# Performance work log

Hardware: AMD Instinct MI355X
Metric: run time of the kernel (lower is better)

The kernel has to match this reference:

```python
import jax, jax.numpy as jnp
import numpy as np

B, C, S, H, W = 2, 128, 64, 128, 512
MID = 32
EPS = 1e-5


def layer_norm(x, g, b):
    m = jnp.mean(x, axis=-1, keepdims=True)
    v = jnp.var(x, axis=-1, keepdims=True)
    return (x - m) / jnp.sqrt(v + EPS) * g + b


def generate_y_for_attn(s, y, u):
    # y: [B, Cy, H, W], u: [B, s, s] int indices into W (clamped)
    b, cy, h, w = y.shape
    u = jnp.clip(u, 0, w - 1)
    yr = y.reshape(b, cy * h, w)
    idx = u.reshape(b, s * s)
    g = jax.vmap(lambda m, i: m[:, i])(yr, idx)          # [B, Cy*H, s^2]
    return g.reshape(b, cy, h, s * s).transpose(0, 3, 2, 1)  # [B, s^2, H, Cy]


def setup_inputs():
    key = jax.random.key(0)
    ks = jax.random.split(key, 10)
    lim = 1.0 / np.sqrt(C)
    return {
        "sat_x": jax.random.normal(ks[0], (B, C, S, S), jnp.float32),
        "grd_x": jax.random.normal(ks[1], (B, C, H, W), jnp.float32),
        "grd_height": jax.random.normal(ks[2], (B, 1, H, W), jnp.float32),
        "u": jax.random.randint(ks[3], (B, S, S), 0, W, jnp.int32),
        "ln_q_g": jnp.ones((C,), jnp.float32),
        "ln_q_b": jnp.zeros((C,), jnp.float32),
        "wq": jax.random.uniform(ks[4], (C, MID), jnp.float32, -lim, lim),
        "bq": jax.random.uniform(ks[5], (MID,), jnp.float32, -lim, lim),
        "ln_k_g": jnp.ones((C,), jnp.float32),
        "ln_k_b": jnp.zeros((C,), jnp.float32),
        "wk": jax.random.uniform(ks[6], (C, MID), jnp.float32, -lim, lim),
        "bk": jax.random.uniform(ks[7], (MID,), jnp.float32, -lim, lim),
    }


def reference(sat_x, grd_x, grd_height, u, ln_q_g, ln_q_b, wq, bq, ln_k_g, ln_k_b, wk, bk):
    b, c, s, _ = sat_x.shape
    scale = MID ** (-0.5)
    y_attn = generate_y_for_attn(s, grd_x, u)        # [B, S^2, H, C]
    v_attn = generate_y_for_attn(s, grd_height, u)   # [B, S^2, H, 1]
    x = sat_x.reshape(b, c, s * s).transpose(0, 2, 1)  # [B, M, C]
    q = layer_norm(x, ln_q_g, ln_q_b) @ wq + bq        # [B, M, 32]
    k = layer_norm(y_attn, ln_k_g, ln_k_b) @ wk + bk   # [B, M, H, 32]
    dot = scale * jnp.einsum("bmd,bmnd->bmn", q, k)    # [B, M, H]
    att = jax.nn.softmax(dot, axis=-1)
    a = jnp.sum(att[..., None] * v_attn, axis=-2)      # [B, M, 1]
    return a.transpose(0, 2, 1).reshape(b, 1, s, s)
```

## Files before the change

### kernel.cpp

```cpp
#include <hip/hip_runtime.h>
#include <math.h>

#define B_   2
#define C_   128
#define S_   64
#define H_   128
#define W_   512
#define M_   (S_ * S_)
#define MID_ 32
#define EPS_ 1e-5f
#define CAP_ 192

#define KBLK (B_ * H_ * (W_ / 64))
#define QBLK (B_ * (M_ / 64))
#define OBLK 4

typedef __attribute__((ext_vector_type(8))) short short8;
typedef __attribute__((ext_vector_type(4))) float floatx4;

__global__ __launch_bounds__(256) void prep_kernel(
    const float* __restrict__ ln_k_g, const float* __restrict__ ln_k_b,
    const float* __restrict__ wk, const float* __restrict__ bk,
    const float* __restrict__ ln_q_g, const float* __restrict__ ln_q_b,
    const float* __restrict__ wq, const float* __restrict__ bq,
    float* __restrict__ prepbuf,
    short* __restrict__ wfrag,
    int* __restrict__ counts,
    int* __restrict__ ocount)
{
    const int tid = threadIdx.x;
    const int blk = blockIdx.x;
    const float* g    = blk ? ln_q_g : ln_k_g;
    const float* bl   = blk ? ln_q_b : ln_k_b;
    const float* wt   = blk ? wq     : wk;
    const float* bias = blk ? bq     : bk;

    __shared__ float pa[256], pb[256];

    float a = 0.f, c2 = 0.f;
#pragma unroll
    for (int k = 0; k < 16; ++k) {
        const int idx = tid + 256 * k;
        const float wv = wt[idx];
        const int c = idx >> 5;
        a  = fmaf(g[c],  wv, a);
        c2 = fmaf(bl[c], wv, c2);
    }
    pa[tid] = a; pb[tid] = c2;

    if (blk == 0) {
        ((int4*)counts)[tid] = make_int4(0, 0, 0, 0);
        if (tid == 0) *ocount = 0;
    }
    __syncthreads();

    if (tid < 32) {
        float s = 0.f, t = 0.f;
#pragma unroll
        for (int r = 0; r < 8; ++r) { s += pa[tid + 32 * r]; t += pb[tid + 32 * r]; }
        prepbuf[blk * 64 + tid]      = s;
        prepbuf[blk * 64 + 32 + tid] = t + bias[tid];
    }

    short* whiT = wfrag + blk * 8192;
    short* wloT = whiT + 4096;
#pragma unroll
    for (int e = 0; e < 16; ++e) {
        const int idx = tid * 16 + e;
        const int i    = idx & 7;
        const int ln   = (idx >> 3) & 63;
        const int kk   = (idx >> 9) & 3;
        const int jt   = idx >> 11;
        const int c = kk * 32 + (ln >> 4) * 8 + i;
        const int j = jt * 16 + (ln & 15);
        const float wp = g[c] * wt[c * MID_ + j];
        const unsigned bbits = __float_as_uint(wp);
        const unsigned hb = bbits & 0xFFFF0000u;
        whiT[idx] = (short)(hb >> 16);
        const float r = wp - __uint_as_float(hb);
        wloT[idx] = (short)(__float_as_uint(r) >> 16);
    }
}

__global__ __launch_bounds__(256) void proj_kernel(
    const float* __restrict__ grd_x,
    const float* __restrict__ sat_x,
    const float* __restrict__ prepbuf,
    const short* __restrict__ wfrag,
    const int*   __restrict__ u,
    float* __restrict__ kw,
    float* __restrict__ qv,
    int* __restrict__ counts,
    int* __restrict__ bucket,
    int* __restrict__ ocount,
    int* __restrict__ olist)
{
    const int tid  = threadIdx.x;
    const int lane = tid & 63;
    const int wv   = __builtin_amdgcn_readfirstlane(tid >> 6);
    const int quad = lane >> 4;
    const int l16  = lane & 15;
    const int blk  = blockIdx.x;
    const bool is_k = (blk < KBLK);

    int b, h = 0, pos0;
    const float* xcol;
    size_t xstr;
    if (is_k) {
        const int wchunk = blk & 7;
        h    = (blk >> 3) & (H_ - 1);
        b    = blk >> 10;
        pos0 = wchunk * 64;
        xcol = grd_x + ((size_t)b * C_ * H_ + h) * W_ + pos0;
        xstr = (size_t)H_ * W_;
    } else {
        const int qblk = blk - KBLK;
        b    = qblk >> 6;
        pos0 = (qblk & 63) * 64;
        xcol = sat_x + (size_t)b * C_ * M_ + pos0;
        xstr = (size_t)M_;
    }
    const int pos = pos0 + wv * 16 + l16;

    const float* xp = xcol + (size_t)(quad * 8) * xstr + wv * 16 + l16;
    float xv[32];
#pragma unroll
    for (int kk = 0; kk < 4; ++kk)
#pragma unroll
        for (int i = 0; i < 8; ++i)
            xv[kk * 8 + i] = xp[(size_t)(kk * 32 + i) * xstr];

    const short* whiT = wfrag + (is_k ? 0 : 8192);
    const short* wloT = whiT + 4096;
    short8 ahi[2][4], alo[2][4];
#pragma unroll
    for (int jt = 0; jt < 2; ++jt)
#pragma unroll
        for (int kk = 0; kk < 4; ++kk) {
            const int off = ((jt * 4 + kk) * 64 + lane) * 8;
            ahi[jt][kk] = *(const short8*)(whiT + off);
            alo[jt][kk] = *(const short8*)(wloT + off);
        }

    const int setoff = is_k ? 0 : 64;
    const float4 gw0 = *(const float4*)(prepbuf + setoff + quad * 4);
    const float4 bw0 = *(const float4*)(prepbuf + setoff + 32 + quad * 4);
    const float4 gw1 = *(const float4*)(prepbuf + setoff + 16 + quad * 4);
    const float4 bw1 = *(const float4*)(prepbuf + setoff + 48 + quad * 4);

    floatx4 acc0 = {0.f, 0.f, 0.f, 0.f};
    floatx4 acc1 = {0.f, 0.f, 0.f, 0.f};
    float p1 = 0.f, p2 = 0.f;

#pragma unroll
    for (int kk = 0; kk < 4; ++kk) {
        union { short8 v; unsigned u[4]; } bhi, blo;
#pragma unroll
        for (int e = 0; e < 4; ++e) {
            const float x0 = xv[kk * 8 + 2 * e];
            const float x1 = xv[kk * 8 + 2 * e + 1];
            p1 += x0 + x1;
            p2 = fmaf(x0, x0, p2);
            p2 = fmaf(x1, x1, p2);
            const unsigned b0 = __float_as_uint(x0);
            const unsigned b1 = __float_as_uint(x1);
            bhi.u[e] = (b1 & 0xFFFF0000u) | (b0 >> 16);
            const float r0 = x0 - __uint_as_float(b0 & 0xFFFF0000u);
            const float r1 = x1 - __uint_as_float(b1 & 0xFFFF0000u);
            blo.u[e] = (__float_as_uint(r1) & 0xFFFF0000u) |
                       (__float_as_uint(r0) >> 16);
        }
        acc0 = __builtin_amdgcn_mfma_f32_16x16x32_bf16(ahi[0][kk], bhi.v, acc0, 0, 0, 0);
        acc1 = __builtin_amdgcn_mfma_f32_16x16x32_bf16(ahi[1][kk], bhi.v, acc1, 0, 0, 0);
        acc0 = __builtin_amdgcn_mfma_f32_16x16x32_bf16(ahi[0][kk], blo.v, acc0, 0, 0, 0);
        acc1 = __builtin_amdgcn_mfma_f32_16x16x32_bf16(ahi[1][kk], blo.v, acc1, 0, 0, 0);
        acc0 = __builtin_amdgcn_mfma_f32_16x16x32_bf16(alo[0][kk], bhi.v, acc0, 0, 0, 0);
        acc1 = __builtin_amdgcn_mfma_f32_16x16x32_bf16(alo[1][kk], bhi.v, acc1, 0, 0, 0);
    }

    p1 += __shfl_xor(p1, 16, 64);
    p1 += __shfl_xor(p1, 32, 64);
    p2 += __shfl_xor(p2, 16, 64);
    p2 += __shfl_xor(p2, 32, 64);
    const float mean = p1 * (1.f / C_);
    const float rstd = rsqrtf(fmaf(-mean, mean, p2 * (1.f / C_)) + EPS_);

    float* orow;
    if (is_k) orow = kw + (((size_t)b * W_ + pos) * H_ + h) * MID_;
    else      orow = qv + ((size_t)b * M_ + pos) * MID_;

    float4 o0, o1;
    o0.x = fmaf(rstd, fmaf(-mean, gw0.x, acc0[0]), bw0.x);
    o0.y = fmaf(rstd, fmaf(-mean, gw0.y, acc0[1]), bw0.y);
    o0.z = fmaf(rstd, fmaf(-mean, gw0.z, acc0[2]), bw0.z);
    o0.w = fmaf(rstd, fmaf(-mean, gw0.w, acc0[3]), bw0.w);
    o1.x = fmaf(rstd, fmaf(-mean, gw1.x, acc1[0]), bw1.x);
    o1.y = fmaf(rstd, fmaf(-mean, gw1.y, acc1[1]), bw1.y);
    o1.z = fmaf(rstd, fmaf(-mean, gw1.z, acc1[2]), bw1.z);
    o1.w = fmaf(rstd, fmaf(-mean, gw1.w, acc1[3]), bw1.w);
    *(float4*)(orow + quad * 4)      = o0;
    *(float4*)(orow + 16 + quad * 4) = o1;

    if (!is_k && quad == 0) {
        const int bm = b * M_ + pos;
        int w = u[bm];
        w = min(max(w, 0), W_ - 1);
        const int bw = b * W_ + w;
        const int p = atomicAdd(&counts[bw], 1);
        if (p < CAP_) bucket[bw * CAP_ + p] = bm;
        else          olist[atomicAdd(ocount, 1)] = bm;
    }
}

__global__ __launch_bounds__(256) void battn_kernel(
    const float* __restrict__ qv,
    const float* __restrict__ kw,
    const float* __restrict__ gh,
    const int*   __restrict__ u,
    const int*   __restrict__ counts,
    const int*   __restrict__ bucket,
    const int*   __restrict__ ocount,
    const int*   __restrict__ olist,
    float* __restrict__ out)
{
    const int blk  = blockIdx.x;
    const int tid  = threadIdx.x;
    const int lane = tid & 63;
    const int wv   = __builtin_amdgcn_readfirstlane(tid >> 6);
    const float sc = 0.17677669529663687f;

    if (blk >= B_ * W_) {
        const int nof = min(*ocount, B_ * M_);
        const int gwv = (blk - B_ * W_) * 4 + wv;
        for (int i = gwv; i < nof; i += OBLK * 4) {
            const int bm = olist[i];
            const int b  = bm >> 12;
            int w = u[bm];
            w = min(max(w, 0), W_ - 1);
            const float4* k4 = (const float4*)(kw + ((size_t)b * W_ + w) * H_ * MID_);
            const float* qr = qv + (size_t)bm * MID_;
            float sq[MID_];
#pragma unroll
            for (int j = 0; j < MID_; ++j) sq[j] = qr[j];
            float d0 = 0.f, d1 = 0.f;
#pragma unroll
            for (int j = 0; j < 8; ++j) {
                const float4 ka = k4[lane * 8 + j];
                const float4 kb = k4[(lane + 64) * 8 + j];
                d0 = fmaf(sq[j*4+0], ka.x, d0); d0 = fmaf(sq[j*4+1], ka.y, d0);
                d0 = fmaf(sq[j*4+2], ka.z, d0); d0 = fmaf(sq[j*4+3], ka.w, d0);
                d1 = fmaf(sq[j*4+0], kb.x, d1); d1 = fmaf(sq[j*4+1], kb.y, d1);
                d1 = fmaf(sq[j*4+2], kb.z, d1); d1 = fmaf(sq[j*4+3], kb.w, d1);
            }
            d0 *= sc; d1 *= sc;
            float mx = fmaxf(d0, d1);
#pragma unroll
            for (int o = 32; o > 0; o >>= 1) mx = fmaxf(mx, __shfl_xor(mx, o, 64));
            const float v0 = gh[((size_t)b * H_ + lane) * W_ + w];
            const float v1 = gh[((size_t)b * H_ + lane + 64) * W_ + w];
            const float e0 = __expf(d0 - mx);
            const float e1 = __expf(d1 - mx);
            float s   = e0 + e1;
            float svv = fmaf(e0, v0, e1 * v1);
#pragma unroll
            for (int o = 32; o > 0; o >>= 1) {
                s   += __shfl_xor(s,   o, 64);
                svv += __shfl_xor(svv, o, 64);
            }
            if (lane == 0) out[bm] = svv / s;
        }
        return;
    }

    const int n = min(counts[blk], CAP_);
    if (wv >= n) return;

    const int b = blk >> 9;
    const int w = blk & (W_ - 1);

    const float4* k4 = (const float4*)(kw + (size_t)blk * H_ * MID_);
    float4 ka[8], kb[8];
#pragma unroll
    for (int j = 0; j < 8; ++j) ka[j] = k4[lane * 8 + j];
#pragma unroll
    for (int j = 0; j < 8; ++j) kb[j] = k4[(lane + 64) * 8 + j];

    const float v0 = gh[((size_t)b * H_ + lane) * W_ + w];
    const float v1 = gh[((size_t)b * H_ + lane + 64) * W_ + w];

    const int* bkt = bucket + (size_t)blk * CAP_;

    for (int i = wv; i < n; i += 4) {
        const int bm = bkt[i];
        const float* qr = qv + (size_t)bm * MID_;
        float sq[MID_];
#pragma unroll
        for (int j = 0; j < MID_; ++j) sq[j] = qr[j];

        float d0 = 0.f, d1 = 0.f;
#pragma unroll
        for (int j = 0; j < 8; ++j) {
            d0 = fmaf(sq[j * 4 + 0], ka[j].x, d0);
            d0 = fmaf(sq[j * 4 + 1], ka[j].y, d0);
            d0 = fmaf(sq[j * 4 + 2], ka[j].z, d0);
            d0 = fmaf(sq[j * 4 + 3], ka[j].w, d0);
            d1 = fmaf(sq[j * 4 + 0], kb[j].x, d1);
            d1 = fmaf(sq[j * 4 + 1], kb[j].y, d1);
            d1 = fmaf(sq[j * 4 + 2], kb[j].z, d1);
            d1 = fmaf(sq[j * 4 + 3], kb[j].w, d1);
        }
        d0 *= sc; d1 *= sc;

        float mx = fmaxf(d0, d1);
#pragma unroll
        for (int o = 32; o > 0; o >>= 1) mx = fmaxf(mx, __shfl_xor(mx, o, 64));

        const float e0 = __expf(d0 - mx);
        const float e1 = __expf(d1 - mx);
        float s   = e0 + e1;
        float svv = fmaf(e0, v0, e1 * v1);
#pragma unroll
        for (int o = 32; o > 0; o >>= 1) {
            s   += __shfl_xor(s,   o, 64);
            svv += __shfl_xor(svv, o, 64);
        }

        if (lane == 0) out[bm] = svv / s;
    }
}

extern "C" void kernel_launch(void* const* d_in, const int* in_sizes, int n_in,
                              void* d_out, int out_size, void* d_ws, size_t ws_size,
                              hipStream_t stream) {
    const float* sat_x      = (const float*)d_in[0];
    const float* grd_x      = (const float*)d_in[1];
    const float* grd_height = (const float*)d_in[2];
    const int*   u          = (const int*)d_in[3];
    const float* ln_q_g     = (const float*)d_in[4];
    const float* ln_q_b     = (const float*)d_in[5];
    const float* wq         = (const float*)d_in[6];
    const float* bq         = (const float*)d_in[7];
    const float* ln_k_g     = (const float*)d_in[8];
    const float* ln_k_b     = (const float*)d_in[9];
    const float* wk         = (const float*)d_in[10];
    const float* bk         = (const float*)d_in[11];

    float* out = (float*)d_out;

    char* ws = (char*)d_ws;
    float* kw      = (float*)ws;
    float* q       = (float*)(ws + (size_t)16 * 1024 * 1024);
    int*   counts  = (int*)  (ws + (size_t)17 * 1024 * 1024);
    int*   ocount  = (int*)  (ws + (size_t)17 * 1024 * 1024 + 4096);
    int*   bucket  = (int*)  (ws + (size_t)17 * 1024 * 1024 + 8192);
    int*   olist   = bucket + B_ * W_ * CAP_;
    float* prepbuf = (float*)(ws + (size_t)18 * 1024 * 1024);
    short* wfrag   = (short*)(ws + (size_t)18 * 1024 * 1024 + 4096);

    prep_kernel<<<2, 256, 0, stream>>>(
        ln_k_g, ln_k_b, wk, bk, ln_q_g, ln_q_b, wq, bq,
        prepbuf, wfrag, counts, ocount);
    proj_kernel<<<KBLK + QBLK, 256, 0, stream>>>(
        grd_x, sat_x, prepbuf, wfrag, u, kw, q, counts, bucket, ocount, olist);
    battn_kernel<<<B_ * W_ + OBLK, 256, 0, stream>>>(
        q, kw, grd_height, u, counts, bucket, ocount, olist, out);
}
```

Measured before the change: 144.6 us.

## Store projected keys as bf16 and stage input tiles via direct global-to-LDS loads

The intermediate key projection buffer is now written in bf16 with round-to-nearest-even instead of fp32. This halves its write traffic in the projection kernel and its read traffic in the attention kernel, which unpacks the values back to fp32. The projection kernel also loads the 128x64 input tile into shared memory with async global_load_lds and an XOR swizzle, replacing strided per-thread register loads, and adds a block barrier. Storing keys in bf16 lowers their precision, so the attention logits may drift slightly from the fp32 reference.

After: 131.8 us, median of 2. 8.8% less time.

```diff
diff --git a/kernel.cpp b/kernel.cpp
--- a/kernel.cpp
+++ b/kernel.cpp
@@ -17,6 +17,12 @@
 
 typedef __attribute__((ext_vector_type(8))) short short8;
 typedef __attribute__((ext_vector_type(4))) float floatx4;
+
+__device__ __forceinline__ unsigned bfpair(float a, float b) {
+    unsigned ua = __float_as_uint(a); ua += 0x7FFFu + ((ua >> 16) & 1u);
+    unsigned ub = __float_as_uint(b); ub += 0x7FFFu + ((ub >> 16) & 1u);
+    return (ua >> 16) | (ub & 0xFFFF0000u);
+}
 
 __global__ __launch_bounds__(256) void prep_kernel(
     const float* __restrict__ ln_k_g, const float* __restrict__ ln_k_b,
@@ -88,13 +94,15 @@
     const float* __restrict__ prepbuf,
     const short* __restrict__ wfrag,
     const int*   __restrict__ u,
-    float* __restrict__ kw,
+    unsigned short* __restrict__ kwb,
     float* __restrict__ qv,
     int* __restrict__ counts,
     int* __restrict__ bucket,
     int* __restrict__ ocount,
     int* __restrict__ olist)
 {
+    __shared__ float xs[C_ * 64];
+
     const int tid  = threadIdx.x;
     const int lane = tid & 63;
     const int wv   = __builtin_amdgcn_readfirstlane(tid >> 6);
@@ -122,13 +130,20 @@
     }
     const int pos = pos0 + wv * 16 + l16;
 
-    const float* xp = xcol + (size_t)(quad * 8) * xstr + wv * 16 + l16;
-    float xv[32];
-#pragma unroll
-    for (int kk = 0; kk < 4; ++kk)
-#pragma unroll
-        for (int i = 0; i < 8; ++i)
-            xv[kk * 8 + i] = xp[(size_t)(kk * 32 + i) * xstr];
+    {
+        const int swz  = (wv >> 1) << 4;
+        const float* gsrc = xcol + (size_t)(lane >> 4) * xstr
+                                 + (((lane & 15) * 4) ^ swz);
+#pragma unroll
+        for (int r = 0; r < 8; ++r) {
+            const float* src = gsrc + (size_t)(r * 16 + wv * 4) * xstr;
+            float* dst = xs + (r * 16 + wv * 4) * 64;
+            __builtin_amdgcn_global_load_lds(
+                (const __attribute__((address_space(1))) unsigned int*)src,
+                (__attribute__((address_space(3))) unsigned int*)dst,
+                16, 0, 0);
+        }
+    }
 
     const short* whiT = wfrag + (is_k ? 0 : 8192);
     const short* wloT = whiT + 4096;
@@ -148,17 +163,23 @@
     const float4 gw1 = *(const float4*)(prepbuf + setoff + 16 + quad * 4);
     const float4 bw1 = *(const float4*)(prepbuf + setoff + 48 + quad * 4);
 
+    __syncthreads();
+
     floatx4 acc0 = {0.f, 0.f, 0.f, 0.f};
     floatx4 acc1 = {0.f, 0.f, 0.f, 0.f};
     float p1 = 0.f, p2 = 0.f;
 
+    const int rpos = (wv * 16 + l16) ^ ((quad & 1) << 4);
+    const float* xsl = xs + quad * 8 * 64 + rpos;
+
 #pragma unroll
     for (int kk = 0; kk < 4; ++kk) {
+        const float* xk = xsl + kk * 32 * 64;
         union { short8 v; unsigned u[4]; } bhi, blo;
 #pragma unroll
         for (int e = 0; e < 4; ++e) {
-            const float x0 = xv[kk * 8 + 2 * e];
-            const float x1 = xv[kk * 8 + 2 * e + 1];
+            const float x0 = xk[(2 * e)     * 64];
+            const float x1 = xk[(2 * e + 1) * 64];
             p1 += x0 + x1;
             p2 = fmaf(x0, x0, p2);
             p2 = fmaf(x1, x1, p2);
@@ -185,36 +206,41 @@
     const float mean = p1 * (1.f / C_);
     const float rstd = rsqrtf(fmaf(-mean, mean, p2 * (1.f / C_)) + EPS_);
 
-    float* orow;
-    if (is_k) orow = kw + (((size_t)b * W_ + pos) * H_ + h) * MID_;
-    else      orow = qv + ((size_t)b * M_ + pos) * MID_;
-
-    float4 o0, o1;
-    o0.x = fmaf(rstd, fmaf(-mean, gw0.x, acc0[0]), bw0.x);
-    o0.y = fmaf(rstd, fmaf(-mean, gw0.y, acc0[1]), bw0.y);
-    o0.z = fmaf(rstd, fmaf(-mean, gw0.z, acc0[2]), bw0.z);
-    o0.w = fmaf(rstd, fmaf(-mean, gw0.w, acc0[3]), bw0.w);
-    o1.x = fmaf(rstd, fmaf(-mean, gw1.x, acc1[0]), bw1.x);
-    o1.y = fmaf(rstd, fmaf(-mean, gw1.y, acc1[1]), bw1.y);
-    o1.z = fmaf(rstd, fmaf(-mean, gw1.z, acc1[2]), bw1.z);
-    o1.w = fmaf(rstd, fmaf(-mean, gw1.w, acc1[3]), bw1.w);
-    *(float4*)(orow + quad * 4)      = o0;
-    *(float4*)(orow + 16 + quad * 4) = o1;
-
-    if (!is_k && quad == 0) {
-        const int bm = b * M_ + pos;
-        int w = u[bm];
-        w = min(max(w, 0), W_ - 1);
-        const int bw = b * W_ + w;
-        const int p = atomicAdd(&counts[bw], 1);
-        if (p < CAP_) bucket[bw * CAP_ + p] = bm;
-        else          olist[atomicAdd(ocount, 1)] = bm;
+    float o0x = fmaf(rstd, fmaf(-mean, gw0.x, acc0[0]), bw0.x);
+    float o0y = fmaf(rstd, fmaf(-mean, gw0.y, acc0[1]), bw0.y);
+    float o0z = fmaf(rstd, fmaf(-mean, gw0.z, acc0[2]), bw0.z);
+    float o0w = fmaf(rstd, fmaf(-mean, gw0.w, acc0[3]), bw0.w);
+    float o1x = fmaf(rstd, fmaf(-mean, gw1.x, acc1[0]), bw1.x);
+    float o1y = fmaf(rstd, fmaf(-mean, gw1.y, acc1[1]), bw1.y);
+    float o1z = fmaf(rstd, fmaf(-mean, gw1.z, acc1[2]), bw1.z);
+    float o1w = fmaf(rstd, fmaf(-mean, gw1.w, acc1[3]), bw1.w);
+
+    if (is_k) {
+        unsigned short* orow = kwb + (((size_t)b * W_ + pos) * H_ + h) * MID_;
+        uint2 u0, u1;
+        u0.x = bfpair(o0x, o0y); u0.y = bfpair(o0z, o0w);
+        u1.x = bfpair(o1x, o1y); u1.y = bfpair(o1z, o1w);
+        *(uint2*)(orow + quad * 4)      = u0;
+        *(uint2*)(orow + 16 + quad * 4) = u1;
+    } else {
+        float* orow = qv + ((size_t)b * M_ + pos) * MID_;
+        *(float4*)(orow + quad * 4)      = make_float4(o0x, o0y, o0z, o0w);
+        *(float4*)(orow + 16 + quad * 4) = make_float4(o1x, o1y, o1z, o1w);
+        if (quad == 0) {
+            const int bm = b * M_ + pos;
+            int w = u[bm];
+            w = min(max(w, 0), W_ - 1);
+            const int bw = b * W_ + w;
+            const int p = atomicAdd(&counts[bw], 1);
+            if (p < CAP_) bucket[bw * CAP_ + p] = bm;
+            else          olist[atomicAdd(ocount, 1)] = bm;
+        }
     }
 }
 
 __global__ __launch_bounds__(256) void battn_kernel(
     const float* __restrict__ qv,
-    const float* __restrict__ kw,
+    const unsigned short* __restrict__ kwb,
     const float* __restrict__ gh,
     const int*   __restrict__ u,
     const int*   __restrict__ counts,
@@ -237,20 +263,16 @@
             const int b  = bm >> 12;
             int w = u[bm];
             w = min(max(w, 0), W_ - 1);
-            const float4* k4 = (const float4*)(kw + ((size_t)b * W_ + w) * H_ * MID_);
+            const unsigned short* kr = kwb + ((size_t)b * W_ + w) * H_ * MID_;
             const float* qr = qv + (size_t)bm * MID_;
             float sq[MID_];
 #pragma unroll
             for (int j = 0; j < MID_; ++j) sq[j] = qr[j];
             float d0 = 0.f, d1 = 0.f;
 #pragma unroll
-            for (int j = 0; j < 8; ++j) {
-                const float4 ka = k4[lane * 8 + j];
-                const float4 kb = k4[(lane + 64) * 8 + j];
-                d0 = fmaf(sq[j*4+0], ka.x, d0); d0 = fmaf(sq[j*4+1], ka.y, d0);
-                d0 = fmaf(sq[j*4+2], ka.z, d0); d0 = fmaf(sq[j*4+3], ka.w, d0);
-                d1 = fmaf(sq[j*4+0], kb.x, d1); d1 = fmaf(sq[j*4+1], kb.y, d1);
-                d1 = fmaf(sq[j*4+2], kb.z, d1); d1 = fmaf(sq[j*4+3], kb.w, d1);
+            for (int j = 0; j < MID_; ++j) {
+                d0 = fmaf(sq[j], __uint_as_float((unsigned)kr[lane * MID_ + j] << 16), d0);
+                d1 = fmaf(sq[j], __uint_as_float((unsigned)kr[(lane + 64) * MID_ + j] << 16), d1);
             }
             d0 *= sc; d1 *= sc;
             float mx = fmaxf(d0, d1);
@@ -278,12 +300,21 @@
     const int b = blk >> 9;
     const int w = blk & (W_ - 1);
 
-    const float4* k4 = (const float4*)(kw + (size_t)blk * H_ * MID_);
-    float4 ka[8], kb[8];
-#pragma unroll
-    for (int j = 0; j < 8; ++j) ka[j] = k4[lane * 8 + j];
-#pragma unroll
-    for (int j = 0; j < 8; ++j) kb[j] = k4[(lane + 64) * 8 + j];
+    const uint4* k4 = (const uint4*)(kwb + (size_t)blk * H_ * MID_);
+    float ka[32], kb[32];
+#pragma unroll
+    for (int t = 0; t < 4; ++t) {
+        const uint4 ua = k4[lane * 4 + t];
+        const uint4 ub = k4[(lane + 64) * 4 + t];
+        ka[t*8+0] = __uint_as_float(ua.x << 16); ka[t*8+1] = __uint_as_float(ua.x & 0xFFFF0000u);
+        ka[t*8+2] = __uint_as_float(ua.y << 16); ka[t*8+3] = __uint_as_float(ua.y & 0xFFFF0000u);
+        ka[t*8+4] = __uint_as_float(ua.z << 16); ka[t*8+5] = __uint_as_float(ua.z & 0xFFFF0000u);
+        ka[t*8+6] = __uint_as_float(ua.w << 16); ka[t*8+7] = __uint_as_float(ua.w & 0xFFFF0000u);
+        kb[t*8+0] = __uint_as_float(ub.x << 16); kb[t*8+1] = __uint_as_float(ub.x & 0xFFFF0000u);
+        kb[t*8+2] = __uint_as_float(ub.y << 16); kb[t*8+3] = __uint_as_float(ub.y & 0xFFFF0000u);
+        kb[t*8+4] = __uint_as_float(ub.z << 16); kb[t*8+5] = __uint_as_float(ub.z & 0xFFFF0000u);
+        kb[t*8+6] = __uint_as_float(ub.w << 16); kb[t*8+7] = __uint_as_float(ub.w & 0xFFFF0000u);
+    }
 
     const float v0 = gh[((size_t)b * H_ + lane) * W_ + w];
     const float v1 = gh[((size_t)b * H_ + lane + 64) * W_ + w];
@@ -299,15 +330,9 @@
 
         float d0 = 0.f, d1 = 0.f;
 #pragma unroll
-        for (int j = 0; j < 8; ++j) {
-            d0 = fmaf(sq[j * 4 + 0], ka[j].x, d0);
-            d0 = fmaf(sq[j * 4 + 1], ka[j].y, d0);
-            d0 = fmaf(sq[j * 4 + 2], ka[j].z, d0);
-            d0 = fmaf(sq[j * 4 + 3], ka[j].w, d0);
-            d1 = fmaf(sq[j * 4 + 0], kb[j].x, d1);
-            d1 = fmaf(sq[j * 4 + 1], kb[j].y, d1);
-            d1 = fmaf(sq[j * 4 + 2], kb[j].z, d1);
-            d1 = fmaf(sq[j * 4 + 3], kb[j].w, d1);
+        for (int j = 0; j < MID_; ++j) {
+            d0 = fmaf(sq[j], ka[j], d0);
+            d1 = fmaf(sq[j], kb[j], d1);
         }
         d0 *= sc; d1 *= sc;
 
@@ -348,20 +373,20 @@
     float* out = (float*)d_out;
 
     char* ws = (char*)d_ws;
-    float* kw      = (float*)ws;
-    float* q       = (float*)(ws + (size_t)16 * 1024 * 1024);
-    int*   counts  = (int*)  (ws + (size_t)17 * 1024 * 1024);
-    int*   ocount  = (int*)  (ws + (size_t)17 * 1024 * 1024 + 4096);
-    int*   bucket  = (int*)  (ws + (size_t)17 * 1024 * 1024 + 8192);
+    unsigned short* kwb = (unsigned short*)ws;
+    float* q       = (float*)(ws + (size_t)8  * 1024 * 1024);
+    int*   counts  = (int*)  (ws + (size_t)9  * 1024 * 1024);
+    int*   ocount  = (int*)  (ws + (size_t)9  * 1024 * 1024 + 4096);
+    int*   bucket  = (int*)  (ws + (size_t)9  * 1024 * 1024 + 8192);
     int*   olist   = bucket + B_ * W_ * CAP_;
-    float* prepbuf = (float*)(ws + (size_t)18 * 1024 * 1024);
-    short* wfrag   = (short*)(ws + (size_t)18 * 1024 * 1024 + 4096);
+    float* prepbuf = (float*)(ws + (size_t)10 * 1024 * 1024);
+    short* wfrag   = (short*)(ws + (size_t)10 * 1024 * 1024 + 4096);
 
     prep_kernel<<<2, 256, 0, stream>>>(
         ln_k_g, ln_k_b, wk, bk, ln_q_g, ln_q_b, wq, bq,
         prepbuf, wfrag, counts, ocount);
     proj_kernel<<<KBLK + QBLK, 256, 0, stream>>>(
-        grd_x, sat_x, prepbuf, wfrag, u, kw, q, counts, bucket, ocount, olist);
+        grd_x, sat_x, prepbuf, wfrag, u, kwb, q, counts, bucket, ocount, olist);
     battn_kernel<<<B_ * W_ + OBLK, 256, 0, stream>>>(
-        q, kw, grd_height, u, counts, bucket, ocount, olist, out);
-}
+        q, kwb, grd_height, u, counts, bucket, ocount, olist, out);
+}
```
